# Kernel tuning notes

Hardware: AMD Instinct MI355X
Metric: run time of the kernel (lower is better)

Reference implementation:

```python
import jax, jax.numpy as jnp
import numpy as np

B, C, H, W = 4, 128, 64, 64


def setup_inputs() -> dict:
    key = jax.random.key(0)
    k1, k2 = jax.random.split(key)
    x = jax.random.normal(k1, (B, C, H, W), dtype=jnp.float32)
    # 1x1 conv kv_mapper: weight [C_out, C_in], bias [C_out]; C_out == C_in == C
    W_kv = jax.random.normal(k2, (C, C), dtype=jnp.float32) * (1.0 / np.sqrt(C))
    b_kv = jnp.zeros((C,), dtype=jnp.float32)
    return {"x": x, "W_kv": W_kv, "b_kv": b_kv}


def reference(x, W_kv, b_kv):
    b, c, h, w = x.shape
    # kv_mapper: 1x1 conv  -> v: [b, c, h, w]
    v = jnp.einsum('bchw,oc->bohw', x, W_kv) + b_kv[None, :, None, None]
    # rearrange 'b c h w -> b (h w) c'
    L = h * w
    values = v.reshape(b, c, L).transpose(0, 2, 1)    # keys == values
    queries = x.reshape(b, c, L).transpose(0, 2, 1)
    # scaled dot-product attention, full [b, L, L] scores
    scores = jnp.einsum('blc,btc->blt', queries, values) / jnp.sqrt(jnp.asarray(c, x.dtype))
    attn = jax.nn.softmax(scores, axis=-1)
    out = jnp.einsum('blt,btv->blv', attn, values)    # [b, L, c]
    # rearrange 'b (h w) c -> b c h w'
    return out.transpose(0, 2, 1).reshape(b, c, h, w)
```

## Files before the change

kernel.cpp:

```cpp
#include <hip/hip_runtime.h>

#define LQ 4096
#define CH 128
#define NB 4
#define QSCALE 0.12753139626233174f
#define MAXCH 8
#define TILE_HW 8192

#if defined(__has_builtin)
#if __has_builtin(__builtin_amdgcn_mfma_f32_16x16x16bf16_1k)
#define HAVE_MFMA16 1
#endif
#endif

typedef __attribute__((ext_vector_type(8))) unsigned short ushort8;
typedef __attribute__((ext_vector_type(4))) unsigned short ushort4v;
typedef __attribute__((ext_vector_type(4))) short short4v;
typedef __attribute__((ext_vector_type(8))) __bf16 bf16x8;
typedef __attribute__((ext_vector_type(4))) float f32x4;

__device__ inline unsigned short f2bf(float f) {
    unsigned int u = __builtin_bit_cast(unsigned int, f);
    u += 0x7fffu + ((u >> 16) & 1u);
    return (unsigned short)(u >> 16);
}
__device__ inline float bf2f(unsigned short h) {
    unsigned int u = (unsigned int)h << 16;
    return __builtin_bit_cast(float, u);
}
__device__ inline unsigned int bfpack2(float a, float b) {
    unsigned int ua = __builtin_bit_cast(unsigned int, a) + 0x8000u;
    unsigned int ub = __builtin_bit_cast(unsigned int, b) + 0x8000u;
    return (ua >> 16) | (ub & 0xffff0000u);
}
__device__ inline void gload_lds16(const unsigned short* g, unsigned short* l) {
    __builtin_amdgcn_global_load_lds(
        (const __attribute__((address_space(1))) unsigned int*)(g),
        (__attribute__((address_space(3))) unsigned int*)(l), 16, 0, 0);
}

__global__ __launch_bounds__(256) void prep_kernel(
    const float* __restrict__ x, const float* __restrict__ Wkv,
    const float* __restrict__ bkv,
    unsigned short* __restrict__ Vt2, unsigned short* __restrict__ Vc2)
{
    __shared__ __align__(16) unsigned short xs[64 * 136];
    __shared__ __align__(16) unsigned short vs[128 * 72];
    const int tid = threadIdx.x;
    const int lane = tid & 63;
    const int wave = tid >> 6;
    const int quad = lane >> 4, l16 = lane & 15;
    const int b = blockIdx.x & 3;
    const int T = blockIdx.x >> 2;
    const int l0 = T << 6;

    {
        const f32x4* xg4 = (const f32x4*)(x + (size_t)b * CH * LQ + l0);
        #pragma unroll
        for (int i = 0; i < 8; ++i) {
            int idx = i * 256 + tid;
            int c = idx >> 4, l4 = idx & 15;
            f32x4 v = xg4[c * (LQ / 4) + l4];
            #pragma unroll
            for (int m = 0; m < 4; ++m) xs[(l4 * 4 + m) * 136 + c] = f2bf(v[m]);
        }
    }
    __syncthreads();

    const int wo = wave * 32;
    f32x4 acc[2][4];
    #pragma unroll
    for (int ot = 0; ot < 2; ++ot)
        #pragma unroll
        for (int lt = 0; lt < 4; ++lt) acc[ot][lt] = f32x4{0.f, 0.f, 0.f, 0.f};

    #pragma unroll
    for (int kc = 0; kc < 4; ++kc) {
        bf16x8 af[2];
        #pragma unroll
        for (int ot = 0; ot < 2; ++ot) {
            const float* wrow = Wkv + (size_t)(wo + ot * 16 + l16) * CH + kc * 32 + quad * 8;
            ushort8 a;
            #pragma unroll
            for (int j = 0; j < 8; ++j) a[j] = f2bf(wrow[j]);
            af[ot] = __builtin_bit_cast(bf16x8, a);
        }
        #pragma unroll
        for (int lt = 0; lt < 4; ++lt) {
            bf16x8 bf = __builtin_bit_cast(bf16x8,
                *(const ushort8*)(xs + (lt * 16 + l16) * 136 + kc * 32 + quad * 8));
            #pragma unroll
            for (int ot = 0; ot < 2; ++ot)
                acc[ot][lt] = __builtin_amdgcn_mfma_f32_16x16x32_bf16(af[ot], bf, acc[ot][lt], 0, 0, 0);
        }
    }
    #pragma unroll
    for (int ot = 0; ot < 2; ++ot) {
        float bias[4];
        #pragma unroll
        for (int r = 0; r < 4; ++r) bias[r] = bkv[wo + ot * 16 + quad * 4 + r];
        #pragma unroll
        for (int lt = 0; lt < 4; ++lt)
            #pragma unroll
            for (int r = 0; r < 4; ++r)
                vs[(wo + ot * 16 + quad * 4 + r) * 72 + lt * 16 + l16] =
                    f2bf(acc[ot][lt][r] + bias[r]);
    }
    __syncthreads();
    const size_t tbase = ((size_t)b * 64 + T) * TILE_HW;
    #pragma unroll
    for (int i = 0; i < 4; ++i) {
        const int ci = i * 256 + tid;
        const int g = ci >> 6, ls = ci & 63;
        const int nt = g >> 2, kc = g & 3, qs = ls >> 4, l16s = ls & 15;
        ushort8 v;
        #pragma unroll
        for (int j = 0; j < 8; ++j) v[j] = vs[(kc * 32 + qs * 8 + j) * 72 + nt * 16 + l16s];
        *(ushort8*)(Vt2 + tbase + (size_t)ci * 8) = v;
    }
    #pragma unroll
    for (int i = 0; i < 4; ++i) {
        const int ci = i * 256 + tid;
        const int g = ci >> 6, ls = ci & 63;
        const int nt = g >> 2, p = g & 3, qs = ls >> 4, l16s = ls & 15;
        ushort4v a = *(const ushort4v*)(vs + (p * 32 + l16s) * 72 + nt * 16 + qs * 4);
        ushort4v c2 = *(const ushort4v*)(vs + (p * 32 + 16 + l16s) * 72 + nt * 16 + qs * 4);
        ushort8 v;
        #pragma unroll
        for (int j = 0; j < 4; ++j) { v[j] = a[j]; v[j + 4] = c2[j]; }
        *(ushort8*)(Vc2 + tbase + (size_t)ci * 8) = v;
    }
}

__global__ __launch_bounds__(256) void attn_kernel(
    const float* __restrict__ x, const unsigned short* __restrict__ Vt2,
    const unsigned short* __restrict__ Vc2,
    unsigned short* __restrict__ Opart, float* __restrict__ Lsum, int titers)
{
    __shared__ __align__(16) unsigned short bufA[2][TILE_HW];
    __shared__ __align__(16) unsigned short bufB[2][TILE_HW];
    const int tid = threadIdx.x;
    const int wave = tid >> 6, lane = tid & 63;
    const int quad = lane >> 4, l16 = lane & 15;
    const int b = blockIdx.x & 3;
    const int rest = blockIdx.x >> 2;
    const int qtile = rest & 31;
    const int chunk = rest >> 5;
    const int q0w = (qtile << 7) + (wave << 5);
    const int Tbase = chunk * titers;

    const unsigned short* vtb = Vt2 + (size_t)b * 64 * TILE_HW;
    const unsigned short* vcb = Vc2 + (size_t)b * 64 * TILE_HW;

    bf16x8 qf[2][4];
    #pragma unroll
    for (int mt = 0; mt < 2; ++mt)
        #pragma unroll
        for (int kc = 0; kc < 4; ++kc) {
            ushort8 v;
            #pragma unroll
            for (int j = 0; j < 8; ++j) {
                int c = kc * 32 + quad * 8 + j;
                v[j] = f2bf(x[((size_t)b * CH + c) * LQ + q0w + mt * 16 + l16] * QSCALE);
            }
            qf[mt][kc] = __builtin_bit_cast(bf16x8, v);
        }

    f32x4 oacc[2][8];
    #pragma unroll
    for (int mt = 0; mt < 2; ++mt)
        #pragma unroll
        for (int i = 0; i < 8; ++i) oacc[mt][i] = f32x4{0.f, 0.f, 0.f, 0.f};
    float lsum[2] = {0.f, 0.f};

    auto issue = [&](int T, int nb) {
        const unsigned short* sa = vtb + (size_t)T * TILE_HW + lane * 8;
        const unsigned short* sb = vcb + (size_t)T * TILE_HW + lane * 8;
        #pragma unroll
        for (int g = 0; g < 4; ++g) {
            const int go = (wave * 4 + g) * 512;
            gload_lds16(sa + go, &bufA[nb][go]);
            gload_lds16(sb + go, &bufB[nb][go]);
        }
    };
    issue(Tbase, 0);

    for (int it = 0; it < titers; ++it) {
        __syncthreads();
        if (it + 1 < titers) issue(Tbase + it + 1, (it + 1) & 1);
        const unsigned short* A = bufA[it & 1];
        const unsigned short* B = bufB[it & 1];
        #pragma unroll
        for (int nt = 0; nt < 4; ++nt) {
            bf16x8 vA[4];
            #pragma unroll
            for (int kc = 0; kc < 4; ++kc)
                vA[kc] = __builtin_bit_cast(bf16x8,
                    *(const ushort8*)(A + (nt * 4 + kc) * 512 + lane * 8));
            f32x4 s[2];
            #pragma unroll
            for (int mt = 0; mt < 2; ++mt) {
                s[mt] = f32x4{0.f, 0.f, 0.f, 0.f};
                #pragma unroll
                for (int kc = 0; kc < 4; ++kc)
                    s[mt] = __builtin_amdgcn_mfma_f32_16x16x32_bf16(vA[kc], qf[mt][kc], s[mt], 0, 0, 0);
            }
#ifdef HAVE_MFMA16
            short4v pf[2];
#else
            bf16x8 pf[2];
#endif
            #pragma unroll
            for (int mt = 0; mt < 2; ++mt) {
                float p0 = __builtin_amdgcn_exp2f(s[mt][0]);
                float p1 = __builtin_amdgcn_exp2f(s[mt][1]);
                float p2 = __builtin_amdgcn_exp2f(s[mt][2]);
                float p3 = __builtin_amdgcn_exp2f(s[mt][3]);
                lsum[mt] += (p0 + p1) + (p2 + p3);
                unsigned int lo = bfpack2(p0, p1);
                unsigned int hi = bfpack2(p2, p3);
#ifdef HAVE_MFMA16
                ushort4v pk;
                pk[0] = (unsigned short)lo; pk[1] = (unsigned short)(lo >> 16);
                pk[2] = (unsigned short)hi; pk[3] = (unsigned short)(hi >> 16);
                pf[mt] = __builtin_bit_cast(short4v, pk);
#else
                ushort8 pk;
                pk[0] = (unsigned short)lo; pk[1] = (unsigned short)(lo >> 16);
                pk[2] = (unsigned short)hi; pk[3] = (unsigned short)(hi >> 16);
                pk[4] = 0; pk[5] = 0; pk[6] = 0; pk[7] = 0;
                pf[mt] = __builtin_bit_cast(bf16x8, pk);
#endif
            }
            #pragma unroll
            for (int p = 0; p < 4; ++p) {
                ushort8 d8 = *(const ushort8*)(B + (nt * 4 + p) * 512 + lane * 8);
                #pragma unroll
                for (int h = 0; h < 2; ++h) {
                    ushort4v f;
                    #pragma unroll
                    for (int j = 0; j < 4; ++j) f[j] = d8[h * 4 + j];
#ifdef HAVE_MFMA16
                    short4v vB = __builtin_bit_cast(short4v, f);
                    #pragma unroll
                    for (int mt = 0; mt < 2; ++mt)
                        oacc[mt][p * 2 + h] = __builtin_amdgcn_mfma_f32_16x16x16bf16_1k(
                            pf[mt], vB, oacc[mt][p * 2 + h], 0, 0, 0);
#else
                    ushort8 vb;
                    #pragma unroll
                    for (int j = 0; j < 4; ++j) { vb[j] = f[j]; vb[j + 4] = 0; }
                    bf16x8 vB = __builtin_bit_cast(bf16x8, vb);
                    #pragma unroll
                    for (int mt = 0; mt < 2; ++mt)
                        oacc[mt][p * 2 + h] = __builtin_amdgcn_mfma_f32_16x16x32_bf16(
                            pf[mt], vB, oacc[mt][p * 2 + h], 0, 0, 0);
#endif
                }
            }
        }
    }
    const size_t pbase = ((size_t)(chunk * NB + b) * LQ);
    #pragma unroll
    for (int mt = 0; mt < 2; ++mt) {
        float v = lsum[mt];
        v += __shfl_xor(v, 16);
        v += __shfl_xor(v, 32);
        if (lane < 16) Lsum[pbase + q0w + mt * 16 + lane] = v;
    }
    #pragma unroll
    for (int mt = 0; mt < 2; ++mt)
        #pragma unroll
        for (int r = 0; r < 4; ++r) {
            const int q = q0w + mt * 16 + quad * 4 + r;
            unsigned short* orow = Opart + (pbase + q) * CH + l16;
            #pragma unroll
            for (int nc = 0; nc < 8; ++nc) orow[nc * 16] = f2bf(oacc[mt][nc][r]);
        }
}

__global__ __launch_bounds__(256) void combine_kernel(
    const unsigned short* __restrict__ Opart, const float* __restrict__ Lsum,
    float* __restrict__ out, int nchunk)
{
    __shared__ __align__(16) float ls[32 * 132];
    __shared__ float linv[32];
    const int tid = threadIdx.x;
    const int b = blockIdx.x & 3;
    const int q0 = (blockIdx.x >> 2) << 5;

    if (tid < 32) {
        float s = 0.f;
        for (int ch = 0; ch < nchunk; ++ch) s += Lsum[(size_t)(ch * NB + b) * LQ + q0 + tid];
        linv[tid] = 1.0f / s;
    }
    __syncthreads();
    {
        const int c8 = (tid & 15) * 8, qg = tid >> 4;
        #pragma unroll
        for (int i = 0; i < 2; ++i) {
            const int q = qg * 2 + i;
            float s[8];
            #pragma unroll
            for (int k = 0; k < 8; ++k) s[k] = 0.f;
            for (int ch = 0; ch < nchunk; ++ch) {
                ushort8 p = *(const ushort8*)(Opart +
                    ((size_t)(ch * NB + b) * LQ + q0 + q) * CH + c8);
                #pragma unroll
                for (int k = 0; k < 8; ++k) s[k] += bf2f(p[k]);
            }
            const float li = linv[q];
            f32x4 o0, o1;
            #pragma unroll
            for (int k = 0; k < 4; ++k) { o0[k] = s[k] * li; o1[k] = s[k + 4] * li; }
            *(f32x4*)(ls + q * 132 + c8) = o0;
            *(f32x4*)(ls + q * 132 + c8 + 4) = o1;
        }
    }
    __syncthreads();
    {
        const int c = tid & 127, qh = tid >> 7;
        float* dst = out + ((size_t)b * CH + c) * LQ + q0 + qh * 16;
        #pragma unroll
        for (int i = 0; i < 4; ++i) {
            f32x4 o;
            #pragma unroll
            for (int r = 0; r < 4; ++r) o[r] = ls[(qh * 16 + i * 4 + r) * 132 + c];
            ((f32x4*)dst)[i] = o;
        }
    }
}

extern "C" void kernel_launch(void* const* d_in, const int* in_sizes, int n_in,
                              void* d_out, int out_size, void* d_ws, size_t ws_size,
                              hipStream_t stream) {
    const float* x   = (const float*)d_in[0];
    const float* Wkv = (const float*)d_in[1];
    const float* bkv = (const float*)d_in[2];
    float* out = (float*)d_out;

    const size_t vElems = (size_t)NB * LQ * CH;
    unsigned short* Vt2 = (unsigned short*)d_ws;
    unsigned short* Vc2 = Vt2 + vElems;
    float* Lsum = (float*)(Vc2 + vElems);
    unsigned short* Opart = (unsigned short*)(Lsum + (size_t)MAXCH * NB * LQ);

    int nchunk = 4;
    const size_t fixed = 2 * vElems * 2 + (size_t)MAXCH * NB * LQ * 4;
    while (nchunk > 1 && fixed + (size_t)nchunk * NB * LQ * CH * 2 > ws_size) nchunk >>= 1;
    const int titers = (LQ / 64) / nchunk;

    prep_kernel<<<dim3(256), dim3(256), 0, stream>>>(x, Wkv, bkv, Vt2, Vc2);
    attn_kernel<<<dim3(128 * nchunk), dim3(256), 0, stream>>>(x, Vt2, Vc2, Opart, Lsum, titers);
    combine_kernel<<<dim3(512), dim3(256), 0, stream>>>(Opart, Lsum, out, nchunk);
}
```

Baseline: 122.4 us.

## Split key dimension across wave pairs with smaller KV tiles and in-block reduction

The attention block now covers 64 queries instead of 128, and its four waves form two query groups times two key halves. Each wave processes 16 keys per 32-key tile, and the two key halves are reduced through LDS at the end. KV tiles shrink to 4096 elements, so the prep layout changes and twice as many blocks launch. The change also raises occupancy via launch bounds, uses setprio around the MFMA sections, and vectorizes the weight loads. Each block now loads K/V for only 64 queries, which doubles K/V tile traffic relative to compute, and the epilogue reduction adds extra LDS work and a barrier.

```diff
diff --git a/kernel.cpp b/kernel.cpp
--- a/kernel.cpp
+++ b/kernel.cpp
@@ -5,7 +5,8 @@
 #define NB 4
 #define QSCALE 0.12753139626233174f
 #define MAXCH 8
-#define TILE_HW 8192
+#define TILE_HW 4096
+#define NTILES 128
 
 #if defined(__has_builtin)
 #if __has_builtin(__builtin_amdgcn_mfma_f32_16x16x16bf16_1k)
@@ -80,9 +81,11 @@
         #pragma unroll
         for (int ot = 0; ot < 2; ++ot) {
             const float* wrow = Wkv + (size_t)(wo + ot * 16 + l16) * CH + kc * 32 + quad * 8;
+            f32x4 w0 = *(const f32x4*)(wrow);
+            f32x4 w1 = *(const f32x4*)(wrow + 4);
             ushort8 a;
             #pragma unroll
-            for (int j = 0; j < 8; ++j) a[j] = f2bf(wrow[j]);
+            for (int j = 0; j < 4; ++j) { a[j] = f2bf(w0[j]); a[j + 4] = f2bf(w1[j]); }
             af[ot] = __builtin_bit_cast(bf16x8, a);
         }
         #pragma unroll
@@ -107,50 +110,51 @@
                     f2bf(acc[ot][lt][r] + bias[r]);
     }
     __syncthreads();
-    const size_t tbase = ((size_t)b * 64 + T) * TILE_HW;
     #pragma unroll
     for (int i = 0; i < 4; ++i) {
         const int ci = i * 256 + tid;
-        const int g = ci >> 6, ls = ci & 63;
+        const int hh = ci >> 9, c9 = ci & 511;
+        const int g = c9 >> 6, ls = c9 & 63;
         const int nt = g >> 2, kc = g & 3, qs = ls >> 4, l16s = ls & 15;
+        const int lt = hh * 32 + nt * 16 + l16s;
         ushort8 v;
         #pragma unroll
-        for (int j = 0; j < 8; ++j) v[j] = vs[(kc * 32 + qs * 8 + j) * 72 + nt * 16 + l16s];
-        *(ushort8*)(Vt2 + tbase + (size_t)ci * 8) = v;
+        for (int j = 0; j < 8; ++j) v[j] = vs[(kc * 32 + qs * 8 + j) * 72 + lt];
+        *(ushort8*)(Vt2 + ((size_t)(b * NTILES + T * 2 + hh)) * TILE_HW + (size_t)c9 * 8) = v;
     }
     #pragma unroll
     for (int i = 0; i < 4; ++i) {
         const int ci = i * 256 + tid;
-        const int g = ci >> 6, ls = ci & 63;
+        const int hh = ci >> 9, c9 = ci & 511;
+        const int g = c9 >> 6, ls = c9 & 63;
         const int nt = g >> 2, p = g & 3, qs = ls >> 4, l16s = ls & 15;
-        ushort4v a = *(const ushort4v*)(vs + (p * 32 + l16s) * 72 + nt * 16 + qs * 4);
-        ushort4v c2 = *(const ushort4v*)(vs + (p * 32 + 16 + l16s) * 72 + nt * 16 + qs * 4);
+        const int t4 = hh * 32 + nt * 16 + qs * 4;
+        ushort4v a = *(const ushort4v*)(vs + (p * 32 + l16s) * 72 + t4);
+        ushort4v c2 = *(const ushort4v*)(vs + (p * 32 + 16 + l16s) * 72 + t4);
         ushort8 v;
         #pragma unroll
         for (int j = 0; j < 4; ++j) { v[j] = a[j]; v[j + 4] = c2[j]; }
-        *(ushort8*)(Vc2 + tbase + (size_t)ci * 8) = v;
-    }
-}
-
-__global__ __launch_bounds__(256) void attn_kernel(
+        *(ushort8*)(Vc2 + ((size_t)(b * NTILES + T * 2 + hh)) * TILE_HW + (size_t)c9 * 8) = v;
+    }
+}
+
+__global__ __launch_bounds__(256, 4) void attn_kernel(
     const float* __restrict__ x, const unsigned short* __restrict__ Vt2,
     const unsigned short* __restrict__ Vc2,
     unsigned short* __restrict__ Opart, float* __restrict__ Lsum, int titers)
 {
-    __shared__ __align__(16) unsigned short bufA[2][TILE_HW];
-    __shared__ __align__(16) unsigned short bufB[2][TILE_HW];
+    __shared__ __align__(16) unsigned short smem[4][TILE_HW];
+    __shared__ __align__(16) float lred[256];
     const int tid = threadIdx.x;
     const int wave = tid >> 6, lane = tid & 63;
     const int quad = lane >> 4, l16 = lane & 15;
+    const int qw = wave & 1, tw = wave >> 1;
     const int b = blockIdx.x & 3;
     const int rest = blockIdx.x >> 2;
-    const int qtile = rest & 31;
-    const int chunk = rest >> 5;
-    const int q0w = (qtile << 7) + (wave << 5);
+    const int qtile = rest & 63;
+    const int chunk = rest >> 6;
+    const int q0w = (qtile << 6) + (qw << 5);
     const int Tbase = chunk * titers;
-
-    const unsigned short* vtb = Vt2 + (size_t)b * 64 * TILE_HW;
-    const unsigned short* vcb = Vc2 + (size_t)b * 64 * TILE_HW;
 
     bf16x8 qf[2][4];
     #pragma unroll
@@ -174,13 +178,13 @@
     float lsum[2] = {0.f, 0.f};
 
     auto issue = [&](int T, int nb) {
-        const unsigned short* sa = vtb + (size_t)T * TILE_HW + lane * 8;
-        const unsigned short* sb = vcb + (size_t)T * TILE_HW + lane * 8;
-        #pragma unroll
-        for (int g = 0; g < 4; ++g) {
-            const int go = (wave * 4 + g) * 512;
-            gload_lds16(sa + go, &bufA[nb][go]);
-            gload_lds16(sb + go, &bufB[nb][go]);
+        const unsigned short* sa = Vt2 + ((size_t)b * NTILES + T) * TILE_HW + lane * 8;
+        const unsigned short* sb = Vc2 + ((size_t)b * NTILES + T) * TILE_HW + lane * 8;
+        #pragma unroll
+        for (int g = 0; g < 2; ++g) {
+            const int go = (wave * 2 + g) * 512;
+            gload_lds16(sa + go, &smem[nb][go]);
+            gload_lds16(sb + go, &smem[2 + nb][go]);
         }
     };
     issue(Tbase, 0);
@@ -188,95 +192,120 @@
     for (int it = 0; it < titers; ++it) {
         __syncthreads();
         if (it + 1 < titers) issue(Tbase + it + 1, (it + 1) & 1);
-        const unsigned short* A = bufA[it & 1];
-        const unsigned short* B = bufB[it & 1];
-        #pragma unroll
-        for (int nt = 0; nt < 4; ++nt) {
-            bf16x8 vA[4];
+        const unsigned short* A = smem[it & 1];
+        const unsigned short* B = smem[2 + (it & 1)];
+        bf16x8 vA[4];
+        #pragma unroll
+        for (int kc = 0; kc < 4; ++kc)
+            vA[kc] = __builtin_bit_cast(bf16x8,
+                *(const ushort8*)(A + (tw * 4 + kc) * 512 + lane * 8));
+        f32x4 s[2];
+        __builtin_amdgcn_s_setprio(1);
+        #pragma unroll
+        for (int mt = 0; mt < 2; ++mt) {
+            s[mt] = f32x4{0.f, 0.f, 0.f, 0.f};
             #pragma unroll
             for (int kc = 0; kc < 4; ++kc)
-                vA[kc] = __builtin_bit_cast(bf16x8,
-                    *(const ushort8*)(A + (nt * 4 + kc) * 512 + lane * 8));
-            f32x4 s[2];
-            #pragma unroll
-            for (int mt = 0; mt < 2; ++mt) {
-                s[mt] = f32x4{0.f, 0.f, 0.f, 0.f};
-                #pragma unroll
-                for (int kc = 0; kc < 4; ++kc)
-                    s[mt] = __builtin_amdgcn_mfma_f32_16x16x32_bf16(vA[kc], qf[mt][kc], s[mt], 0, 0, 0);
-            }
+                s[mt] = __builtin_amdgcn_mfma_f32_16x16x32_bf16(vA[kc], qf[mt][kc], s[mt], 0, 0, 0);
+        }
+        __builtin_amdgcn_s_setprio(0);
 #ifdef HAVE_MFMA16
-            short4v pf[2];
+        short4v pf[2];
 #else
-            bf16x8 pf[2];
-#endif
-            #pragma unroll
-            for (int mt = 0; mt < 2; ++mt) {
-                float p0 = __builtin_amdgcn_exp2f(s[mt][0]);
-                float p1 = __builtin_amdgcn_exp2f(s[mt][1]);
-                float p2 = __builtin_amdgcn_exp2f(s[mt][2]);
-                float p3 = __builtin_amdgcn_exp2f(s[mt][3]);
-                lsum[mt] += (p0 + p1) + (p2 + p3);
-                unsigned int lo = bfpack2(p0, p1);
-                unsigned int hi = bfpack2(p2, p3);
+        bf16x8 pf[2];
+#endif
+        #pragma unroll
+        for (int mt = 0; mt < 2; ++mt) {
+            float p0 = __builtin_amdgcn_exp2f(s[mt][0]);
+            float p1 = __builtin_amdgcn_exp2f(s[mt][1]);
+            float p2 = __builtin_amdgcn_exp2f(s[mt][2]);
+            float p3 = __builtin_amdgcn_exp2f(s[mt][3]);
+            lsum[mt] += (p0 + p1) + (p2 + p3);
+            unsigned int lo = bfpack2(p0, p1);
+            unsigned int hi = bfpack2(p2, p3);
 #ifdef HAVE_MFMA16
-                ushort4v pk;
-                pk[0] = (unsigned short)lo; pk[1] = (unsigned short)(lo >> 16);
-                pk[2] = (unsigned short)hi; pk[3] = (unsigned short)(hi >> 16);
-                pf[mt] = __builtin_bit_cast(short4v, pk);
+            ushort4v pk;
+            pk[0] = (unsigned short)lo; pk[1] = (unsigned short)(lo >> 16);
+            pk[2] = (unsigned short)hi; pk[3] = (unsigned short)(hi >> 16);
+            pf[mt] = __builtin_bit_cast(short4v, pk);
 #else
-                ushort8 pk;
-                pk[0] = (unsigned short)lo; pk[1] = (unsigned short)(lo >> 16);
-                pk[2] = (unsigned short)hi; pk[3] = (unsigned short)(hi >> 16);
-                pk[4] = 0; pk[5] = 0; pk[6] = 0; pk[7] = 0;
-                pf[mt] = __builtin_bit_cast(bf16x8, pk);
-#endif
-            }
-            #pragma unroll
-            for (int p = 0; p < 4; ++p) {
-                ushort8 d8 = *(const ushort8*)(B + (nt * 4 + p) * 512 + lane * 8);
-                #pragma unroll
-                for (int h = 0; h < 2; ++h) {
-                    ushort4v f;
-                    #pragma unroll
-                    for (int j = 0; j < 4; ++j) f[j] = d8[h * 4 + j];
+            ushort8 pk;
+            pk[0] = (unsigned short)lo; pk[1] = (unsigned short)(lo >> 16);
+            pk[2] = (unsigned short)hi; pk[3] = (unsigned short)(hi >> 16);
+            pk[4] = 0; pk[5] = 0; pk[6] = 0; pk[7] = 0;
+            pf[mt] = __builtin_bit_cast(bf16x8, pk);
+#endif
+        }
+        __builtin_amdgcn_s_setprio(1);
+        #pragma unroll
+        for (int p = 0; p < 4; ++p) {
+            ushort8 d8 = *(const ushort8*)(B + (tw * 4 + p) * 512 + lane * 8);
+            #pragma unroll
+            for (int h = 0; h < 2; ++h) {
+                ushort4v f;
+                #pragma unroll
+                for (int j = 0; j < 4; ++j) f[j] = d8[h * 4 + j];
 #ifdef HAVE_MFMA16
-                    short4v vB = __builtin_bit_cast(short4v, f);
-                    #pragma unroll
-                    for (int mt = 0; mt < 2; ++mt)
-                        oacc[mt][p * 2 + h] = __builtin_amdgcn_mfma_f32_16x16x16bf16_1k(
-                            pf[mt], vB, oacc[mt][p * 2 + h], 0, 0, 0);
+                short4v vB = __builtin_bit_cast(short4v, f);
+                #pragma unroll
+                for (int mt = 0; mt < 2; ++mt)
+                    oacc[mt][p * 2 + h] = __builtin_amdgcn_mfma_f32_16x16x16bf16_1k(
+                        pf[mt], vB, oacc[mt][p * 2 + h], 0, 0, 0);
 #else
-                    ushort8 vb;
-                    #pragma unroll
-                    for (int j = 0; j < 4; ++j) { vb[j] = f[j]; vb[j + 4] = 0; }
-                    bf16x8 vB = __builtin_bit_cast(bf16x8, vb);
-                    #pragma unroll
-                    for (int mt = 0; mt < 2; ++mt)
-                        oacc[mt][p * 2 + h] = __builtin_amdgcn_mfma_f32_16x16x32_bf16(
-                            pf[mt], vB, oacc[mt][p * 2 + h], 0, 0, 0);
-#endif
-                }
-            }
-        }
-    }
-    const size_t pbase = ((size_t)(chunk * NB + b) * LQ);
-    #pragma unroll
-    for (int mt = 0; mt < 2; ++mt) {
-        float v = lsum[mt];
-        v += __shfl_xor(v, 16);
-        v += __shfl_xor(v, 32);
-        if (lane < 16) Lsum[pbase + q0w + mt * 16 + lane] = v;
-    }
-    #pragma unroll
-    for (int mt = 0; mt < 2; ++mt)
-        #pragma unroll
-        for (int r = 0; r < 4; ++r) {
-            const int q = q0w + mt * 16 + quad * 4 + r;
-            unsigned short* orow = Opart + (pbase + q) * CH + l16;
-            #pragma unroll
-            for (int nc = 0; nc < 8; ++nc) orow[nc * 16] = f2bf(oacc[mt][nc][r]);
-        }
+                ushort8 vb;
+                #pragma unroll
+                for (int j = 0; j < 4; ++j) { vb[j] = f[j]; vb[j + 4] = 0; }
+                bf16x8 vB = __builtin_bit_cast(bf16x8, vb);
+                #pragma unroll
+                for (int mt = 0; mt < 2; ++mt)
+                    oacc[mt][p * 2 + h] = __builtin_amdgcn_mfma_f32_16x16x32_bf16(
+                        pf[mt], vB, oacc[mt][p * 2 + h], 0, 0, 0);
+#endif
+            }
+        }
+        __builtin_amdgcn_s_setprio(0);
+    }
+
+    __syncthreads();
+    float* red = (float*)smem;
+    if (tw == 1) {
+        #pragma unroll
+        for (int mt = 0; mt < 2; ++mt) {
+            #pragma unroll
+            for (int nc = 0; nc < 8; ++nc)
+                *(f32x4*)(red + qw * 4096 + (mt * 8 + nc) * 256 + lane * 4) = oacc[mt][nc];
+            lred[qw * 128 + mt * 64 + lane] = lsum[mt];
+        }
+    }
+    __syncthreads();
+    if (tw == 0) {
+        #pragma unroll
+        for (int mt = 0; mt < 2; ++mt) {
+            #pragma unroll
+            for (int nc = 0; nc < 8; ++nc) {
+                f32x4 t = *(const f32x4*)(red + qw * 4096 + (mt * 8 + nc) * 256 + lane * 4);
+                oacc[mt][nc] += t;
+            }
+            lsum[mt] += lred[qw * 128 + mt * 64 + lane];
+        }
+        const size_t pbase = ((size_t)(chunk * NB + b) * LQ);
+        #pragma unroll
+        for (int mt = 0; mt < 2; ++mt) {
+            float v = lsum[mt];
+            v += __shfl_xor(v, 16);
+            v += __shfl_xor(v, 32);
+            if (lane < 16) Lsum[pbase + q0w + mt * 16 + lane] = v;
+        }
+        #pragma unroll
+        for (int mt = 0; mt < 2; ++mt)
+            #pragma unroll
+            for (int r = 0; r < 4; ++r) {
+                const int q = q0w + mt * 16 + quad * 4 + r;
+                unsigned short* orow = Opart + (pbase + q) * CH + l16;
+                #pragma unroll
+                for (int nc = 0; nc < 8; ++nc) orow[nc * 16] = f2bf(oacc[mt][nc][r]);
+            }
+    }
 }
 
 __global__ __launch_bounds__(256) void combine_kernel(
@@ -348,9 +377,9 @@
     int nchunk = 4;
     const size_t fixed = 2 * vElems * 2 + (size_t)MAXCH * NB * LQ * 4;
     while (nchunk > 1 && fixed + (size_t)nchunk * NB * LQ * CH * 2 > ws_size) nchunk >>= 1;
-    const int titers = (LQ / 64) / nchunk;
+    const int titers = (LQ / 32) / nchunk;
 
     prep_kernel<<<dim3(256), dim3(256), 0, stream>>>(x, Wkv, bkv, Vt2, Vc2);
-    attn_kernel<<<dim3(128 * nchunk), dim3(256), 0, stream>>>(x, Vt2, Vc2, Opart, Lsum, titers);
+    attn_kernel<<<dim3(256 * nchunk), dim3(256), 0, stream>>>(x, Vt2, Vc2, Opart, Lsum, titers);
     combine_kernel<<<dim3(512), dim3(256), 0, stream>>>(Opart, Lsum, out, nchunk);
 }
```

Measured after the change: 129.8 us. 6.1% more time.

## Restructure attention loop into split-phase single-buffered K/V loads with priority hints

Applied to the files above, without the earlier changes.

The double-buffered K and V tiles in LDS become single buffers. The V tile is now loaded while the scores and exp are computed from K, and the next K tile is loaded while the PV MFMAs run, with explicit vmcnt waits and barriers between the phases. This halves LDS use so three blocks can fit per CU, and occupancy is hinted via launch_bounds. It also adds s_setprio around the MFMA sections, doubles the number of key-chunks for more parallelism, and vectorizes the weight loads in the prep kernel. The risks are a second barrier per iteration, higher register pressure from keeping all P fragments live, and a larger partial-output combine cost.

```diff
diff --git a/kernel.cpp b/kernel.cpp
--- a/kernel.cpp
+++ b/kernel.cpp
@@ -80,9 +80,11 @@
         #pragma unroll
         for (int ot = 0; ot < 2; ++ot) {
             const float* wrow = Wkv + (size_t)(wo + ot * 16 + l16) * CH + kc * 32 + quad * 8;
+            f32x4 w0 = *(const f32x4*)(wrow);
+            f32x4 w1 = *(const f32x4*)(wrow + 4);
             ushort8 a;
             #pragma unroll
-            for (int j = 0; j < 8; ++j) a[j] = f2bf(wrow[j]);
+            for (int j = 0; j < 4; ++j) { a[j] = f2bf(w0[j]); a[j + 4] = f2bf(w1[j]); }
             af[ot] = __builtin_bit_cast(bf16x8, a);
         }
         #pragma unroll
@@ -132,13 +134,13 @@
     }
 }
 
-__global__ __launch_bounds__(256) void attn_kernel(
+__global__ __launch_bounds__(256, 3) void attn_kernel(
     const float* __restrict__ x, const unsigned short* __restrict__ Vt2,
     const unsigned short* __restrict__ Vc2,
     unsigned short* __restrict__ Opart, float* __restrict__ Lsum, int titers)
 {
-    __shared__ __align__(16) unsigned short bufA[2][TILE_HW];
-    __shared__ __align__(16) unsigned short bufB[2][TILE_HW];
+    __shared__ __align__(16) unsigned short bufA[TILE_HW];
+    __shared__ __align__(16) unsigned short bufB[TILE_HW];
     const int tid = threadIdx.x;
     const int wave = tid >> 6, lane = tid & 63;
     const int quad = lane >> 4, l16 = lane & 15;
@@ -173,31 +175,43 @@
         for (int i = 0; i < 8; ++i) oacc[mt][i] = f32x4{0.f, 0.f, 0.f, 0.f};
     float lsum[2] = {0.f, 0.f};
 
-    auto issue = [&](int T, int nb) {
+    auto issueA = [&](int T) {
         const unsigned short* sa = vtb + (size_t)T * TILE_HW + lane * 8;
-        const unsigned short* sb = vcb + (size_t)T * TILE_HW + lane * 8;
         #pragma unroll
         for (int g = 0; g < 4; ++g) {
             const int go = (wave * 4 + g) * 512;
-            gload_lds16(sa + go, &bufA[nb][go]);
-            gload_lds16(sb + go, &bufB[nb][go]);
+            gload_lds16(sa + go, &bufA[go]);
         }
     };
-    issue(Tbase, 0);
+    auto issueB = [&](int T) {
+        const unsigned short* sb = vcb + (size_t)T * TILE_HW + lane * 8;
+        #pragma unroll
+        for (int g = 0; g < 4; ++g) {
+            const int go = (wave * 4 + g) * 512;
+            gload_lds16(sb + go, &bufB[go]);
+        }
+    };
+    issueA(Tbase);
 
     for (int it = 0; it < titers; ++it) {
-        __syncthreads();
-        if (it + 1 < titers) issue(Tbase + it + 1, (it + 1) & 1);
-        const unsigned short* A = bufA[it & 1];
-        const unsigned short* B = bufB[it & 1];
+        asm volatile("s_waitcnt vmcnt(0)" ::: "memory");
+        __builtin_amdgcn_s_barrier();
+        issueB(Tbase + it);
+
+#ifdef HAVE_MFMA16
+        short4v pf[4][2];
+#else
+        bf16x8 pf[4][2];
+#endif
         #pragma unroll
         for (int nt = 0; nt < 4; ++nt) {
             bf16x8 vA[4];
             #pragma unroll
             for (int kc = 0; kc < 4; ++kc)
                 vA[kc] = __builtin_bit_cast(bf16x8,
-                    *(const ushort8*)(A + (nt * 4 + kc) * 512 + lane * 8));
+                    *(const ushort8*)(bufA + (nt * 4 + kc) * 512 + lane * 8));
             f32x4 s[2];
+            __builtin_amdgcn_s_setprio(1);
             #pragma unroll
             for (int mt = 0; mt < 2; ++mt) {
                 s[mt] = f32x4{0.f, 0.f, 0.f, 0.f};
@@ -205,11 +219,7 @@
                 for (int kc = 0; kc < 4; ++kc)
                     s[mt] = __builtin_amdgcn_mfma_f32_16x16x32_bf16(vA[kc], qf[mt][kc], s[mt], 0, 0, 0);
             }
-#ifdef HAVE_MFMA16
-            short4v pf[2];
-#else
-            bf16x8 pf[2];
-#endif
+            __builtin_amdgcn_s_setprio(0);
             #pragma unroll
             for (int mt = 0; mt < 2; ++mt) {
                 float p0 = __builtin_amdgcn_exp2f(s[mt][0]);
@@ -223,18 +233,27 @@
                 ushort4v pk;
                 pk[0] = (unsigned short)lo; pk[1] = (unsigned short)(lo >> 16);
                 pk[2] = (unsigned short)hi; pk[3] = (unsigned short)(hi >> 16);
-                pf[mt] = __builtin_bit_cast(short4v, pk);
+                pf[nt][mt] = __builtin_bit_cast(short4v, pk);
 #else
                 ushort8 pk;
                 pk[0] = (unsigned short)lo; pk[1] = (unsigned short)(lo >> 16);
                 pk[2] = (unsigned short)hi; pk[3] = (unsigned short)(hi >> 16);
                 pk[4] = 0; pk[5] = 0; pk[6] = 0; pk[7] = 0;
-                pf[mt] = __builtin_bit_cast(bf16x8, pk);
-#endif
-            }
+                pf[nt][mt] = __builtin_bit_cast(bf16x8, pk);
+#endif
+            }
+        }
+
+        asm volatile("s_waitcnt vmcnt(0)" ::: "memory");
+        __builtin_amdgcn_s_barrier();
+        if (it + 1 < titers) issueA(Tbase + it + 1);
+
+        __builtin_amdgcn_s_setprio(1);
+        #pragma unroll
+        for (int nt = 0; nt < 4; ++nt) {
             #pragma unroll
             for (int p = 0; p < 4; ++p) {
-                ushort8 d8 = *(const ushort8*)(B + (nt * 4 + p) * 512 + lane * 8);
+                ushort8 d8 = *(const ushort8*)(bufB + (nt * 4 + p) * 512 + lane * 8);
                 #pragma unroll
                 for (int h = 0; h < 2; ++h) {
                     ushort4v f;
@@ -245,7 +264,7 @@
                     #pragma unroll
                     for (int mt = 0; mt < 2; ++mt)
                         oacc[mt][p * 2 + h] = __builtin_amdgcn_mfma_f32_16x16x16bf16_1k(
-                            pf[mt], vB, oacc[mt][p * 2 + h], 0, 0, 0);
+                            pf[nt][mt], vB, oacc[mt][p * 2 + h], 0, 0, 0);
 #else
                     ushort8 vb;
                     #pragma unroll
@@ -254,11 +273,12 @@
                     #pragma unroll
                     for (int mt = 0; mt < 2; ++mt)
                         oacc[mt][p * 2 + h] = __builtin_amdgcn_mfma_f32_16x16x32_bf16(
-                            pf[mt], vB, oacc[mt][p * 2 + h], 0, 0, 0);
+                            pf[nt][mt], vB, oacc[mt][p * 2 + h], 0, 0, 0);
 #endif
                 }
             }
         }
+        __builtin_amdgcn_s_setprio(0);
     }
     const size_t pbase = ((size_t)(chunk * NB + b) * LQ);
     #pragma unroll
@@ -345,7 +365,7 @@
     float* Lsum = (float*)(Vc2 + vElems);
     unsigned short* Opart = (unsigned short*)(Lsum + (size_t)MAXCH * NB * LQ);
 
-    int nchunk = 4;
+    int nchunk = 8;
     const size_t fixed = 2 * vElems * 2 + (size_t)MAXCH * NB * LQ * 4;
     while (nchunk > 1 && fixed + (size_t)nchunk * NB * LQ * CH * 2 > ws_size) nchunk >>= 1;
     const int titers = (LQ / 64) / nchunk;
```

Result: no change. 124.4 us (+1.7%).
